# Optimization experiments

Measured on AMD Instinct MI355X. Metric: run time of the kernel, lower is better.

Reference implementation:

```python
import jax, jax.numpy as jnp
import numpy as np

N_NODES = 100000
N_EDGES = 1600000
DIM = 128
N_LAYERS = 3
N_GRAPHS = 512
BN_EPS = 1e-5


def setup_inputs() -> dict:
    key = jax.random.key(0)
    ks = jax.random.split(key, 8)
    x = jax.random.normal(ks[0], (N_NODES, DIM), dtype=jnp.float32)
    edge_index = jax.random.randint(ks[1], (2, N_EDGES), 0, N_NODES)
    batch = jnp.sort(jax.random.randint(ks[2], (N_NODES,), 0, N_GRAPHS))
    s = 1.0 / np.sqrt(DIM).astype(np.float32)
    # GIN MLP per layer: Linear(DIM->DIM), ReLU, Linear(DIM->DIM); stacked over layers
    W1 = jax.random.normal(ks[3], (N_LAYERS, DIM, DIM), dtype=jnp.float32) * s
    b1 = jnp.zeros((N_LAYERS, DIM), jnp.float32)
    W2 = jax.random.normal(ks[4], (N_LAYERS, DIM, DIM), dtype=jnp.float32) * s
    b2 = jnp.zeros((N_LAYERS, DIM), jnp.float32)
    # BatchNorm1d affine params
    gamma = jnp.ones((N_LAYERS, DIM), jnp.float32)
    beta = jnp.zeros((N_LAYERS, DIM), jnp.float32)
    return dict(x=x, edge_index=edge_index, batch=batch,
                W1=W1, b1=b1, W2=W2, b2=b2, gamma=gamma, beta=beta)


def reference(x, edge_index, batch, W1, b1, W2, b2, gamma, beta):
    src, dst = edge_index[0], edge_index[1]
    n = x.shape[0]
    z = x
    zs = []
    for l in range(N_LAYERS):
        # GINConv (eps=0): h_i = MLP((1+eps)*z_i + sum_{j in N(i)} z_j)
        agg = jax.ops.segment_sum(z[src], dst, num_segments=n)  # scatter-add messages
        h = agg + z
        h = jnp.maximum(h @ W1[l] + b1[l], 0.0) @ W2[l] + b2[l]
        h = jnp.maximum(h, 0.0)  # F.relu
        # BatchNorm1d (training-mode batch statistics, biased variance)
        mu = h.mean(axis=0)
        var = h.var(axis=0)
        z = (h - mu) * jax.lax.rsqrt(var + BN_EPS) * gamma[l] + beta[l]
        zs.append(z)
    gs = [jax.ops.segment_sum(zl, batch, num_segments=N_GRAPHS) for zl in zs]
    z_out = jnp.concatenate(zs, axis=1)   # [N, L*DIM]
    g_out = jnp.concatenate(gs, axis=1)   # [G, L*DIM]
    return (z_out, g_out)
```

## Files before the change

kernel.cpp:

```cpp
#include <hip/hip_runtime.h>

#define N_NODES 100000
#define N_EDGES 1600000
#define DIM 128
#define NLAYERS 3
#define NGRAPHS 512
#define BN_EPS 1e-5f

#define SCHUNK 512
#define SBLOCKS ((N_NODES + SCHUNK - 1) / SCHUNK)

#define WPL 5120
#define WCH 10240
#define LSTRIDE 81920

#define NRANGE 8
#define RNODES (N_NODES / NRANGE)

typedef __attribute__((ext_vector_type(8))) short short8;
typedef __attribute__((ext_vector_type(4))) float f32x4;

__device__ __forceinline__ unsigned f2b(float f) {
  unsigned u = __float_as_uint(f);
  return (u + 0x7FFFu + ((u >> 16) & 1u)) >> 16;
}
__device__ __forceinline__ float b2f(unsigned hw) {
  return __uint_as_float(hw << 16);
}

__global__ __launch_bounds__(256) void hist_kernel(const int* __restrict__ dst,
                                                   int* __restrict__ deg) {
  for (int e = blockIdx.x * blockDim.x + threadIdx.x; e < N_EDGES;
       e += gridDim.x * blockDim.x)
    atomicAdd(&deg[dst[e]], 1);
}

__global__ __launch_bounds__(256) void partial_kernel(const int* __restrict__ deg,
                                                      int* __restrict__ bsum) {
  __shared__ int red[256];
  const int t = threadIdx.x;
  const int i0 = blockIdx.x * SCHUNK + 2 * t;
  int s = 0;
  if (i0 + 1 < N_NODES) {
    const int2 v = *(const int2*)(deg + i0);
    s = v.x + v.y;
  } else if (i0 < N_NODES) {
    s = deg[i0];
  }
  red[t] = s;
  __syncthreads();
  for (int off = 128; off > 0; off >>= 1) {
    if (t < off) red[t] += red[t + off];
    __syncthreads();
  }
  if (t == 0) bsum[blockIdx.x] = red[0];
}

__global__ __launch_bounds__(256) void bscan_kernel(const int* __restrict__ bsum,
                                                    int* __restrict__ boff,
                                                    int* __restrict__ row_ptr) {
  __shared__ int s[256];
  const int t = threadIdx.x;
  const int v = (t < SBLOCKS) ? bsum[t] : 0;
  s[t] = v;
  __syncthreads();
  for (int off = 1; off < 256; off <<= 1) {
    int u = (t >= off) ? s[t - off] : 0;
    __syncthreads();
    s[t] += u;
    __syncthreads();
  }
  if (t < SBLOCKS) boff[t] = s[t] - v;
  if (t == SBLOCKS - 1) row_ptr[N_NODES] = s[t];
}

__global__ __launch_bounds__(256) void emit_kernel(const int* __restrict__ deg,
                                                   const int* __restrict__ boff,
                                                   int* __restrict__ row_ptr,
                                                   int* __restrict__ cursor) {
  __shared__ int s[256];
  const int t = threadIdx.x;
  const int i0 = blockIdx.x * SCHUNK + 2 * t;
  int d0 = 0, d1 = 0;
  if (i0 + 1 < N_NODES) {
    const int2 v = *(const int2*)(deg + i0);
    d0 = v.x; d1 = v.y;
  } else if (i0 < N_NODES) {
    d0 = deg[i0];
  }
  const int pair = d0 + d1;
  s[t] = pair;
  __syncthreads();
  for (int off = 1; off < 256; off <<= 1) {
    int u = (t >= off) ? s[t - off] : 0;
    __syncthreads();
    s[t] += u;
    __syncthreads();
  }
  const int base = boff[blockIdx.x] + s[t] - pair;
  if (i0 + 1 < N_NODES) {
    const int2 rp = make_int2(base, base + d0);
    *(int2*)(row_ptr + i0) = rp;
    *(int2*)(cursor + i0) = rp;
  } else if (i0 < N_NODES) {
    row_ptr[i0] = base;
    cursor[i0] = base;
  }
}

__global__ __launch_bounds__(256) void fill_kernel(const int* __restrict__ src,
                                                   const int* __restrict__ dst,
                                                   int* __restrict__ cursor,
                                                   int* __restrict__ col) {
  const int r = blockIdx.x & (NRANGE - 1);
  const int lo = r * RNODES;
  const int hi = lo + RNODES;
  const int nb = gridDim.x >> 3;
  const int bi = blockIdx.x >> 3;
  for (int e = bi * 256 + threadIdx.x; e < N_EDGES; e += nb * 256) {
    const int d = dst[e];
    if (d >= lo && d < hi) {
      const int pos = atomicAdd(&cursor[d], 1);
      col[pos] = src[e];
    }
  }
}

__global__ __launch_bounds__(256) void xcvt_kernel(const float* __restrict__ x,
                                                   ushort* __restrict__ zb) {
  const int i = blockIdx.x * 256 + threadIdx.x;
  const float4 a = ((const float4*)x)[2 * i];
  const float4 b = ((const float4*)x)[2 * i + 1];
  uint4 o;
  o.x = (f2b(a.y) << 16) | f2b(a.x);
  o.y = (f2b(a.w) << 16) | f2b(a.z);
  o.z = (f2b(b.y) << 16) | f2b(b.x);
  o.w = (f2b(b.w) << 16) | f2b(b.z);
  ((uint4*)zb)[i] = o;
}

__global__ __launch_bounds__(256) void wcvt_kernel(const float* __restrict__ W1,
                                                   const float* __restrict__ W2,
                                                   ushort* __restrict__ wsplit) {
  const int id = blockIdx.x * 256 + threadIdx.x;
  const int n = id & 127;
  const int kk = (id >> 7) & 31;
  const int kc = (id >> 12) & 3;
  const int p = (id >> 14) & 1;
  const int l = id >> 15;
  const float* src = p ? W2 : W1;
  const float v = src[(size_t)l * 16384 + (kc * 32 + kk) * 128 + n];
  const unsigned hi = f2b(v);
  const unsigned lo = f2b(v - b2f(hi));
  ushort* dst = wsplit + (size_t)((l * 2 + p) * 4 + kc) * WCH + n * 40 + kk;
  dst[0] = (ushort)hi;
  dst[WPL] = (ushort)lo;
}

__global__ __launch_bounds__(256) void agg_kernel(const ushort* __restrict__ zb,
                                                  const int* __restrict__ row_ptr,
                                                  const int* __restrict__ col,
                                                  ushort* __restrict__ aggh,
                                                  ushort* __restrict__ aggl) {
  const int w = (blockIdx.x * 256 + threadIdx.x) >> 6;
  const int lane = threadIdx.x & 63;
  if (w >= N_NODES) return;
  const int start = row_ptr[w];
  const int end = row_ptr[w + 1];

  const unsigned us = ((const unsigned*)(zb + (size_t)w * 128))[lane];
  float ax = b2f(us & 0xFFFFu), ay = b2f(us >> 16);
  int j = start;
  for (; j + 8 <= end; j += 8) {
    const int c0 = col[j], c1 = col[j + 1], c2 = col[j + 2], c3 = col[j + 3];
    const int c4 = col[j + 4], c5 = col[j + 5], c6 = col[j + 6], c7 = col[j + 7];
    const unsigned u0 = ((const unsigned*)(zb + (size_t)c0 * 128))[lane];
    const unsigned u1 = ((const unsigned*)(zb + (size_t)c1 * 128))[lane];
    const unsigned u2 = ((const unsigned*)(zb + (size_t)c2 * 128))[lane];
    const unsigned u3 = ((const unsigned*)(zb + (size_t)c3 * 128))[lane];
    const unsigned u4 = ((const unsigned*)(zb + (size_t)c4 * 128))[lane];
    const unsigned u5 = ((const unsigned*)(zb + (size_t)c5 * 128))[lane];
    const unsigned u6 = ((const unsigned*)(zb + (size_t)c6 * 128))[lane];
    const unsigned u7 = ((const unsigned*)(zb + (size_t)c7 * 128))[lane];
    ax += ((b2f(u0 & 0xFFFFu) + b2f(u1 & 0xFFFFu)) + (b2f(u2 & 0xFFFFu) + b2f(u3 & 0xFFFFu))) +
          ((b2f(u4 & 0xFFFFu) + b2f(u5 & 0xFFFFu)) + (b2f(u6 & 0xFFFFu) + b2f(u7 & 0xFFFFu)));
    ay += ((b2f(u0 >> 16) + b2f(u1 >> 16)) + (b2f(u2 >> 16) + b2f(u3 >> 16))) +
          ((b2f(u4 >> 16) + b2f(u5 >> 16)) + (b2f(u6 >> 16) + b2f(u7 >> 16)));
  }
  for (; j + 4 <= end; j += 4) {
    const int c0 = col[j], c1 = col[j + 1], c2 = col[j + 2], c3 = col[j + 3];
    const unsigned u0 = ((const unsigned*)(zb + (size_t)c0 * 128))[lane];
    const unsigned u1 = ((const unsigned*)(zb + (size_t)c1 * 128))[lane];
    const unsigned u2 = ((const unsigned*)(zb + (size_t)c2 * 128))[lane];
    const unsigned u3 = ((const unsigned*)(zb + (size_t)c3 * 128))[lane];
    ax += (b2f(u0 & 0xFFFFu) + b2f(u1 & 0xFFFFu)) + (b2f(u2 & 0xFFFFu) + b2f(u3 & 0xFFFFu));
    ay += (b2f(u0 >> 16) + b2f(u1 >> 16)) + (b2f(u2 >> 16) + b2f(u3 >> 16));
  }
  for (; j < end; ++j) {
    const unsigned uc = ((const unsigned*)(zb + (size_t)col[j] * 128))[lane];
    ax += b2f(uc & 0xFFFFu);
    ay += b2f(uc >> 16);
  }
  const unsigned hx = f2b(ax), hy = f2b(ay);
  const unsigned lx = f2b(ax - b2f(hx)), ly = f2b(ay - b2f(hy));
  ((unsigned*)(aggh + (size_t)w * 128))[lane] = (hy << 16) | hx;
  ((unsigned*)(aggl + (size_t)w * 128))[lane] = (ly << 16) | lx;
}

__global__ __launch_bounds__(256) void mlp_kernel(
    const ushort* __restrict__ Xhp,
    const ushort* __restrict__ Xlp,
    const ushort* __restrict__ Wsp,
    const float* __restrict__ b1,
    const float* __restrict__ b2,
    float* __restrict__ out,
    int lcol,
    float* __restrict__ bnsum) {
  __shared__ __align__(16) ushort smem[2 * 64 * 136 + WCH];
  ushort* Xh = smem;
  ushort* Xl = smem + 64 * 136;
  ushort* Wc = smem + 2 * 64 * 136;
  float* red = (float*)smem;

  const int tid = threadIdx.x;
  const int l = tid & 63, wv = tid >> 6;
  const int lr = l & 15, lg = l >> 4;
  const int n0 = blockIdx.x * 64;

  for (int i = tid; i < 64 * 16; i += 256) {
    const int row = i >> 4, ch = i & 15;
    int4 vh = make_int4(0, 0, 0, 0), vl = vh;
    if (n0 + row < N_NODES) {
      vh = *(const int4*)(Xhp + (size_t)(n0 + row) * 128 + ch * 8);
      vl = *(const int4*)(Xlp + (size_t)(n0 + row) * 128 + ch * 8);
    }
    *(int4*)(Xh + row * 136 + ch * 8) = vh;
    *(int4*)(Xl + row * 136 + ch * 8) = vl;
  }

  f32x4 acc[8];
#pragma unroll
  for (int p = 0; p < 2; ++p) {
#pragma unroll
    for (int nt = 0; nt < 8; ++nt) acc[nt] = {0.f, 0.f, 0.f, 0.f};
#pragma unroll
    for (int kc = 0; kc < 4; ++kc) {
      __syncthreads();
      {
        const uint4* wsrc = (const uint4*)(Wsp + (size_t)(p * 4 + kc) * WCH);
        for (int i = tid; i < WCH / 8; i += 256) ((uint4*)Wc)[i] = wsrc[i];
      }
      __syncthreads();
      const short8 ah = *(const short8*)(Xh + (wv * 16 + lr) * 136 + kc * 32 + lg * 8);
      const short8 al = *(const short8*)(Xl + (wv * 16 + lr) * 136 + kc * 32 + lg * 8);
#pragma unroll
      for (int nt = 0; nt < 8; ++nt) {
        const short8 bh = *(const short8*)(Wc + (nt * 16 + lr) * 40 + lg * 8);
        const short8 bl = *(const short8*)(Wc + WPL + (nt * 16 + lr) * 40 + lg * 8);
        acc[nt] = __builtin_amdgcn_mfma_f32_16x16x32_bf16(ah, bh, acc[nt], 0, 0, 0);
        acc[nt] = __builtin_amdgcn_mfma_f32_16x16x32_bf16(al, bh, acc[nt], 0, 0, 0);
        acc[nt] = __builtin_amdgcn_mfma_f32_16x16x32_bf16(ah, bl, acc[nt], 0, 0, 0);
      }
    }
    if (p == 0) {
      __syncthreads();
      float b1v[8];
#pragma unroll
      for (int nt = 0; nt < 8; ++nt) b1v[nt] = b1[nt * 16 + lr];
#pragma unroll
      for (int nt = 0; nt < 8; ++nt) {
#pragma unroll
        for (int r = 0; r < 4; ++r) {
          const float h = fmaxf(acc[nt][r] + b1v[nt], 0.f);
          const unsigned hi = f2b(h);
          const unsigned lo = f2b(h - b2f(hi));
          Xh[(wv * 16 + lg * 4 + r) * 136 + nt * 16 + lr] = (ushort)hi;
          Xl[(wv * 16 + lg * 4 + r) * 136 + nt * 16 + lr] = (ushort)lo;
        }
      }
    }
  }

  float s[8], q2[8];
  {
    float b2v[8];
#pragma unroll
    for (int nt = 0; nt < 8; ++nt) b2v[nt] = b2[nt * 16 + lr];
#pragma unroll
    for (int nt = 0; nt < 8; ++nt) { s[nt] = 0.f; q2[nt] = 0.f; }
#pragma unroll
    for (int nt = 0; nt < 8; ++nt) {
#pragma unroll
      for (int r = 0; r < 4; ++r) {
        const int n = n0 + wv * 16 + lg * 4 + r;
        const float h = fmaxf(acc[nt][r] + b2v[nt], 0.f);
        if (n < N_NODES) {
          out[(size_t)n * (NLAYERS * DIM) + lcol + nt * 16 + lr] = h;
          s[nt] += h;
          q2[nt] += h * h;
        }
      }
    }
  }
  __syncthreads();

  const int rg = tid >> 4, cb = tid & 15;
#pragma unroll
  for (int nt = 0; nt < 8; ++nt) red[rg * 128 + nt * 16 + cb] = s[nt];
  __syncthreads();
  if (tid < 128) {
    float t = 0.f;
#pragma unroll
    for (int g = 0; g < 16; ++g) t += red[g * 128 + tid];
    unsafeAtomicAdd(&bnsum[tid], t);
  }
  __syncthreads();
#pragma unroll
  for (int nt = 0; nt < 8; ++nt) red[rg * 128 + nt * 16 + cb] = q2[nt];
  __syncthreads();
  if (tid < 128) {
    float t = 0.f;
#pragma unroll
    for (int g = 0; g < 16; ++g) t += red[g * 128 + tid];
    unsafeAtomicAdd(&bnsum[128 + tid], t);
  }
}

__global__ __launch_bounds__(128) void bn_finalize_kernel(
    const float* __restrict__ bnsum, const float* __restrict__ gamma,
    const float* __restrict__ beta, float* __restrict__ bnfin) {
  const int c = threadIdx.x;
  const float inv_n = 1.f / (float)N_NODES;
  const float mu = bnsum[c] * inv_n;
  const float var = bnsum[128 + c] * inv_n - mu * mu;
  const float inv = rsqrtf(var + BN_EPS);
  const float sc = gamma[c] * inv;
  bnfin[c] = sc;
  bnfin[128 + c] = beta[c] - mu * sc;
}

__global__ __launch_bounds__(256) void bn_norm_kernel(float* __restrict__ zcol,
                                                      const float* __restrict__ bnfin,
                                                      ushort* __restrict__ zb) {
  const int idx = blockIdx.x * 256 + threadIdx.x;
  if (idx >= N_NODES * 32) return;
  const int n = idx >> 5, c4 = idx & 31;
  const float4 sc = ((const float4*)bnfin)[c4];
  const float4 sh = ((const float4*)(bnfin + 128))[c4];
  float4* p = (float4*)(zcol + (size_t)n * (NLAYERS * DIM)) + c4;
  float4 v = *p;
  v.x = fmaf(v.x, sc.x, sh.x);
  v.y = fmaf(v.y, sc.y, sh.y);
  v.z = fmaf(v.z, sc.z, sh.z);
  v.w = fmaf(v.w, sc.w, sh.w);
  *p = v;
  if (zb) {
    uint2 o;
    o.x = (f2b(v.y) << 16) | f2b(v.x);
    o.y = (f2b(v.w) << 16) | f2b(v.z);
    *(uint2*)(zb + (size_t)n * 128 + c4 * 4) = o;
  }
}

__global__ __launch_bounds__(128) void pool_kernel(const float* __restrict__ zout,
                                                   const int* __restrict__ batch,
                                                   float* __restrict__ gout) {
  const int g = blockIdx.x / 3;
  const int chunk = blockIdx.x % 3;
  const int c = chunk * 128 + threadIdx.x;
  int lo = 0, hi = N_NODES;
  while (lo < hi) {
    const int m = (lo + hi) >> 1;
    if (batch[m] < g) lo = m + 1; else hi = m;
  }
  int lo2 = lo, hi2 = N_NODES;
  while (lo2 < hi2) {
    const int m = (lo2 + hi2) >> 1;
    if (batch[m] < g + 1) lo2 = m + 1; else hi2 = m;
  }
  float acc = 0.f;
  for (int n = lo; n < lo2; ++n) acc += zout[(size_t)n * (NLAYERS * DIM) + c];
  gout[(size_t)g * (NLAYERS * DIM) + c] = acc;
}

extern "C" void kernel_launch(void* const* d_in, const int* in_sizes, int n_in,
                              void* d_out, int out_size, void* d_ws, size_t ws_size,
                              hipStream_t stream) {
  const float* x = (const float*)d_in[0];
  const int* ei = (const int*)d_in[1];
  const int* src = ei;
  const int* dst = ei + N_EDGES;
  const int* batch = (const int*)d_in[2];
  const float* W1 = (const float*)d_in[3];
  const float* b1 = (const float*)d_in[4];
  const float* W2 = (const float*)d_in[5];
  const float* b2 = (const float*)d_in[6];
  const float* gamma = (const float*)d_in[7];
  const float* beta = (const float*)d_in[8];
  float* out = (float*)d_out;
  float* gout = out + (size_t)N_NODES * NLAYERS * DIM;

  char* ws = (char*)d_ws;
  size_t off = 0;
  auto alloc = [&](size_t bytes) -> void* {
    off = (off + 511) & ~(size_t)511;
    void* p = ws + off;
    off += bytes;
    return p;
  };
  int* row_ptr = (int*)alloc((N_NODES + 1) * sizeof(int));
  int* cursor = (int*)alloc(N_NODES * sizeof(int));
  int* deg = (int*)alloc(N_NODES * sizeof(int));
  int* col = (int*)alloc(N_EDGES * sizeof(int));
  int* bsum = (int*)alloc(SBLOCKS * sizeof(int));
  int* boff = (int*)alloc(SBLOCKS * sizeof(int));
  ushort* zb = (ushort*)alloc((size_t)N_NODES * 128 * sizeof(ushort));
  ushort* aggh = (ushort*)alloc((size_t)N_NODES * 128 * sizeof(ushort));
  ushort* aggl = (ushort*)alloc((size_t)N_NODES * 128 * sizeof(ushort));
  ushort* wsplit = (ushort*)alloc((size_t)NLAYERS * LSTRIDE * sizeof(ushort));
  float* bnsum = (float*)alloc(NLAYERS * 256 * sizeof(float));
  float* bnfin = (float*)alloc(NLAYERS * 256 * sizeof(float));

  hipMemsetAsync(deg, 0, N_NODES * sizeof(int), stream);
  hipMemsetAsync(bnsum, 0, NLAYERS * 256 * sizeof(float), stream);

  hist_kernel<<<2048, 256, 0, stream>>>(dst, deg);
  partial_kernel<<<SBLOCKS, 256, 0, stream>>>(deg, bsum);
  bscan_kernel<<<1, 256, 0, stream>>>(bsum, boff, row_ptr);
  emit_kernel<<<SBLOCKS, 256, 0, stream>>>(deg, boff, row_ptr, cursor);
  fill_kernel<<<2048, 256, 0, stream>>>(src, dst, cursor, col);
  xcvt_kernel<<<(N_NODES * DIM / 8) / 256, 256, 0, stream>>>(x, zb);
  wcvt_kernel<<<384, 256, 0, stream>>>(W1, W2, wsplit);

  for (int l = 0; l < NLAYERS; ++l) {
    agg_kernel<<<(N_NODES * 64 + 255) / 256, 256, 0, stream>>>(zb, row_ptr, col,
                                                               aggh, aggl);
    mlp_kernel<<<(N_NODES + 63) / 64, 256, 0, stream>>>(
        aggh, aggl, wsplit + (size_t)l * LSTRIDE, b1 + (size_t)l * DIM,
        b2 + (size_t)l * DIM, out, l * DIM, bnsum + l * 256);
    bn_finalize_kernel<<<1, 128, 0, stream>>>(bnsum + l * 256, gamma + l * DIM,
                                              beta + l * DIM, bnfin + l * 256);
    bn_norm_kernel<<<(N_NODES * 32 + 255) / 256, 256, 0, stream>>>(
        out + (size_t)l * DIM, bnfin + l * 256, (l < NLAYERS - 1) ? zb : nullptr);
  }
  pool_kernel<<<NGRAPHS * 3, 128, 0, stream>>>(out, batch, gout);
}
```

Before: 966.9 us.

## Read MLP operands directly from global memory instead of staging through LDS

The MLP kernel no longer copies weight chunks and input tiles into shared memory with block-wide barriers. Each lane now loads its A and B MFMA fragments straight from global memory (weights stay L2/L1 resident), and the weight layout becomes a simple transposed n-major plane to suit this. Only the hidden activation still passes through LDS. Launch bounds now request 4 blocks per CU. This removes the per-chunk __syncthreads and staging copies. In exchange, redundant global and L1 traffic for the weights rises, because every wave reloads them.

```diff
diff --git a/kernel.cpp b/kernel.cpp
--- a/kernel.cpp
+++ b/kernel.cpp
@@ -10,9 +10,8 @@
 #define SCHUNK 512
 #define SBLOCKS ((N_NODES + SCHUNK - 1) / SCHUNK)
 
-#define WPL 5120
-#define WCH 10240
-#define LSTRIDE 81920
+#define WPLANE 16384
+#define LSTRIDE (4 * WPLANE)
 
 #define NRANGE 8
 #define RNODES (N_NODES / NRANGE)
@@ -143,18 +142,17 @@
                                                    const float* __restrict__ W2,
                                                    ushort* __restrict__ wsplit) {
   const int id = blockIdx.x * 256 + threadIdx.x;
-  const int n = id & 127;
-  const int kk = (id >> 7) & 31;
-  const int kc = (id >> 12) & 3;
+  const int k = id & 127;
+  const int n = (id >> 7) & 127;
   const int p = (id >> 14) & 1;
   const int l = id >> 15;
   const float* src = p ? W2 : W1;
-  const float v = src[(size_t)l * 16384 + (kc * 32 + kk) * 128 + n];
+  const float v = src[(size_t)l * WPLANE + k * 128 + n];
   const unsigned hi = f2b(v);
   const unsigned lo = f2b(v - b2f(hi));
-  ushort* dst = wsplit + (size_t)((l * 2 + p) * 4 + kc) * WCH + n * 40 + kk;
+  ushort* dst = wsplit + (size_t)l * LSTRIDE + (size_t)p * 2 * WPLANE + n * 128 + k;
   dst[0] = (ushort)hi;
-  dst[WPL] = (ushort)lo;
+  dst[WPLANE] = (ushort)lo;
 }
 
 __global__ __launch_bounds__(256) void agg_kernel(const ushort* __restrict__ zb,
@@ -207,7 +205,7 @@
   ((unsigned*)(aggl + (size_t)w * 128))[lane] = (ly << 16) | lx;
 }
 
-__global__ __launch_bounds__(256) void mlp_kernel(
+__global__ __launch_bounds__(256, 4) void mlp_kernel(
     const ushort* __restrict__ Xhp,
     const ushort* __restrict__ Xlp,
     const ushort* __restrict__ Wsp,
@@ -216,84 +214,87 @@
     float* __restrict__ out,
     int lcol,
     float* __restrict__ bnsum) {
-  __shared__ __align__(16) ushort smem[2 * 64 * 136 + WCH];
-  ushort* Xh = smem;
-  ushort* Xl = smem + 64 * 136;
-  ushort* Wc = smem + 2 * 64 * 136;
+  __shared__ __align__(16) ushort smem[2 * 64 * 136];
+  ushort* Hh = smem;
+  ushort* Hl = smem + 64 * 136;
   float* red = (float*)smem;
 
   const int tid = threadIdx.x;
   const int l = tid & 63, wv = tid >> 6;
   const int lr = l & 15, lg = l >> 4;
   const int n0 = blockIdx.x * 64;
-
-  for (int i = tid; i < 64 * 16; i += 256) {
-    const int row = i >> 4, ch = i & 15;
-    int4 vh = make_int4(0, 0, 0, 0), vl = vh;
-    if (n0 + row < N_NODES) {
-      vh = *(const int4*)(Xhp + (size_t)(n0 + row) * 128 + ch * 8);
-      vl = *(const int4*)(Xlp + (size_t)(n0 + row) * 128 + ch * 8);
-    }
-    *(int4*)(Xh + row * 136 + ch * 8) = vh;
-    *(int4*)(Xl + row * 136 + ch * 8) = vl;
-  }
+  const int arow = min(n0 + wv * 16 + lr, N_NODES - 1);
+  const size_t abase = (size_t)arow * 128 + lg * 8;
+  const int bbase = lr * 128 + lg * 8;
 
   f32x4 acc[8];
 #pragma unroll
-  for (int p = 0; p < 2; ++p) {
-#pragma unroll
-    for (int nt = 0; nt < 8; ++nt) acc[nt] = {0.f, 0.f, 0.f, 0.f};
+  for (int nt = 0; nt < 8; ++nt) acc[nt] = {0.f, 0.f, 0.f, 0.f};
+
+  {
+    const ushort* Wh = Wsp;
+    const ushort* Wl = Wsp + WPLANE;
 #pragma unroll
     for (int kc = 0; kc < 4; ++kc) {
-      __syncthreads();
-      {
-        const uint4* wsrc = (const uint4*)(Wsp + (size_t)(p * 4 + kc) * WCH);
-        for (int i = tid; i < WCH / 8; i += 256) ((uint4*)Wc)[i] = wsrc[i];
-      }
-      __syncthreads();
-      const short8 ah = *(const short8*)(Xh + (wv * 16 + lr) * 136 + kc * 32 + lg * 8);
-      const short8 al = *(const short8*)(Xl + (wv * 16 + lr) * 136 + kc * 32 + lg * 8);
+      const short8 ah = *(const short8*)(Xhp + abase + kc * 32);
+      const short8 al = *(const short8*)(Xlp + abase + kc * 32);
 #pragma unroll
       for (int nt = 0; nt < 8; ++nt) {
-        const short8 bh = *(const short8*)(Wc + (nt * 16 + lr) * 40 + lg * 8);
-        const short8 bl = *(const short8*)(Wc + WPL + (nt * 16 + lr) * 40 + lg * 8);
+        const short8 bh = *(const short8*)(Wh + nt * 2048 + bbase + kc * 32);
+        const short8 bl = *(const short8*)(Wl + nt * 2048 + bbase + kc * 32);
         acc[nt] = __builtin_amdgcn_mfma_f32_16x16x32_bf16(ah, bh, acc[nt], 0, 0, 0);
         acc[nt] = __builtin_amdgcn_mfma_f32_16x16x32_bf16(al, bh, acc[nt], 0, 0, 0);
         acc[nt] = __builtin_amdgcn_mfma_f32_16x16x32_bf16(ah, bl, acc[nt], 0, 0, 0);
       }
     }
-    if (p == 0) {
-      __syncthreads();
-      float b1v[8];
-#pragma unroll
-      for (int nt = 0; nt < 8; ++nt) b1v[nt] = b1[nt * 16 + lr];
+  }
+
+  {
+#pragma unroll
+    for (int nt = 0; nt < 8; ++nt) {
+      const float b1v = b1[nt * 16 + lr];
+#pragma unroll
+      for (int r = 0; r < 4; ++r) {
+        const float h = fmaxf(acc[nt][r] + b1v, 0.f);
+        const unsigned hi = f2b(h);
+        const unsigned lo = f2b(h - b2f(hi));
+        Hh[(wv * 16 + lg * 4 + r) * 136 + nt * 16 + lr] = (ushort)hi;
+        Hl[(wv * 16 + lg * 4 + r) * 136 + nt * 16 + lr] = (ushort)lo;
+      }
+      acc[nt] = {0.f, 0.f, 0.f, 0.f};
+    }
+  }
+
+  {
+    const ushort* Wh = Wsp + 2 * WPLANE;
+    const ushort* Wl = Wsp + 3 * WPLANE;
+    const int hrow = (wv * 16 + lr) * 136 + lg * 8;
+#pragma unroll
+    for (int kc = 0; kc < 4; ++kc) {
+      const short8 ah = *(const short8*)(Hh + hrow + kc * 32);
+      const short8 al = *(const short8*)(Hl + hrow + kc * 32);
 #pragma unroll
       for (int nt = 0; nt < 8; ++nt) {
-#pragma unroll
-        for (int r = 0; r < 4; ++r) {
-          const float h = fmaxf(acc[nt][r] + b1v[nt], 0.f);
-          const unsigned hi = f2b(h);
-          const unsigned lo = f2b(h - b2f(hi));
-          Xh[(wv * 16 + lg * 4 + r) * 136 + nt * 16 + lr] = (ushort)hi;
-          Xl[(wv * 16 + lg * 4 + r) * 136 + nt * 16 + lr] = (ushort)lo;
-        }
+        const short8 bh = *(const short8*)(Wh + nt * 2048 + bbase + kc * 32);
+        const short8 bl = *(const short8*)(Wl + nt * 2048 + bbase + kc * 32);
+        acc[nt] = __builtin_amdgcn_mfma_f32_16x16x32_bf16(ah, bh, acc[nt], 0, 0, 0);
+        acc[nt] = __builtin_amdgcn_mfma_f32_16x16x32_bf16(al, bh, acc[nt], 0, 0, 0);
+        acc[nt] = __builtin_amdgcn_mfma_f32_16x16x32_bf16(ah, bl, acc[nt], 0, 0, 0);
       }
     }
   }
 
   float s[8], q2[8];
   {
-    float b2v[8];
-#pragma unroll
-    for (int nt = 0; nt < 8; ++nt) b2v[nt] = b2[nt * 16 + lr];
 #pragma unroll
     for (int nt = 0; nt < 8; ++nt) { s[nt] = 0.f; q2[nt] = 0.f; }
 #pragma unroll
     for (int nt = 0; nt < 8; ++nt) {
+      const float b2v = b2[nt * 16 + lr];
 #pragma unroll
       for (int r = 0; r < 4; ++r) {
         const int n = n0 + wv * 16 + lg * 4 + r;
-        const float h = fmaxf(acc[nt][r] + b2v[nt], 0.f);
+        const float h = fmaxf(acc[nt][r] + b2v, 0.f);
         if (n < N_NODES) {
           out[(size_t)n * (NLAYERS * DIM) + lcol + nt * 16 + lr] = h;
           s[nt] += h;
```

Result: slower. 1.089 ms (+12.6%).
